# Performance work log

Measured on AMD Instinct MI355X. Metric: run time of the kernel, lower is better.

## Reference

```python
import jax, jax.numpy as jnp
import numpy as np

N_NODES = 100000
IN_CH, HID_CH, OUT_CH = 128, 128, 64
N_EDGES = 1600000


def _gcn_conv(x, W, b, src, dst, num_nodes):
    """PyG GCNConv with gcn_norm(add_self_loops=True): adds one self-loop per
    node to the given edge set, symmetric deg^-1/2 normalization, then
    gather-scale-scatter of the linearly transformed features."""
    loop = jnp.arange(num_nodes)
    s = jnp.concatenate([src, loop])
    d = jnp.concatenate([dst, loop])
    # degree over targets (flow source_to_target), edge weights = 1
    deg = jax.ops.segment_sum(jnp.ones_like(s, x.dtype), d, num_segments=num_nodes)
    dinv = jnp.where(deg > 0, deg ** -0.5, 0.0)
    norm = dinv[s] * dinv[d]                      # [E']
    h = x @ W                                     # [N, out]
    msg = h[s] * norm[:, None]                    # [E', out] gather + scale
    out = jax.ops.segment_sum(msg, d, num_segments=num_nodes)  # scatter-add
    return out + b


def setup_inputs() -> dict:
    key = jax.random.key(0)
    k = jax.random.split(key, 6)
    x = jax.random.normal(k[0], (N_NODES, IN_CH), dtype=jnp.float32)
    edge_index = jax.random.randint(k[1], (2, N_EDGES), 0, N_NODES, dtype=jnp.int64)
    # Glorot-scale params
    W1 = jax.random.normal(k[2], (IN_CH, HID_CH), dtype=jnp.float32) * (2.0 / (IN_CH + HID_CH)) ** 0.5
    b1 = jnp.zeros((HID_CH,), dtype=jnp.float32)
    W2 = jax.random.normal(k[3], (HID_CH, OUT_CH), dtype=jnp.float32) * (2.0 / (HID_CH + OUT_CH)) ** 0.5
    b2 = jnp.zeros((OUT_CH,), dtype=jnp.float32)
    return {"x": x, "edge_index": edge_index, "W1": W1, "b1": b1, "W2": W2, "b2": b2}


def reference(x, edge_index, W1, b1, W2, b2):
    num_nodes = x.shape[0]
    loop = jnp.arange(num_nodes, dtype=edge_index.dtype)
    # wrapper-level add_self_loops (GCNConv adds another internally)
    src = jnp.concatenate([edge_index[0], loop])
    dst = jnp.concatenate([edge_index[1], loop])
    h = _gcn_conv(x, W1, b1, src, dst, num_nodes)
    h = jax.nn.relu(h)
    h = _gcn_conv(h, W2, b2, src, dst, num_nodes)
    return jax.nn.log_softmax(h, axis=1)
```

## Files before the change

kernel.cpp:

```cpp
#include <hip/hip_runtime.h>
#include <cstdint>
#include <cstddef>

#define IN_CH 128
#define HID_CH 128
#define OUT_CH 64
#define BSH 8
#define PB 4096

typedef unsigned int uint32;
typedef unsigned char uchar;
typedef short bf16x8 __attribute__((ext_vector_type(8)));
typedef float f32x4 __attribute__((ext_vector_type(4)));
typedef float f32x2 __attribute__((ext_vector_type(2)));

static __device__ __forceinline__ unsigned short f2bf(float f) {
    uint32 u = __float_as_uint(f);
    u += 0x7fffu + ((u >> 16) & 1u);
    return (unsigned short)(u >> 16);
}
static __device__ __forceinline__ uchar f2fp8(float f) {
    int p = __builtin_amdgcn_cvt_pk_fp8_f32(f, f, 0, false);
    return (uchar)(p & 0xff);
}


__global__ __launch_bounds__(256) void bhist_wtrans(
    const int* __restrict__ dst, int* __restrict__ bcnt, int E, int NB, int gP,
    const float* __restrict__ W1, const float* __restrict__ W2,
    unsigned short* __restrict__ W1t, unsigned short* __restrict__ W2t) {
    if (blockIdx.x >= (uint32)gP) {
        int t = (blockIdx.x - gP) * 256 + threadIdx.x;
        if (t < 128 * 128) {
            int nc = t >> 7, k = t & 127;
            W1t[t] = f2bf(W1[k * 128 + nc]);
        }
        int u = t - 128 * 128;
        if (u >= 0 && u < 64 * 128) {
            int nc = u >> 7, k = u & 127;
            W2t[u] = f2bf(W2[k * 64 + nc]);
        }
        return;
    }
    __shared__ int h[512];
    int t = threadIdx.x;
    int e0 = blockIdx.x * PB;
    int cnt = min(PB, E - e0);
    for (int b = t; b < NB; b += 256) h[b] = 0;
    __syncthreads();
    for (int i = t; i < cnt; i += 256)
        atomicAdd(&h[dst[e0 + i] >> BSH], 1);
    __syncthreads();
    for (int b = t; b < NB; b += 256)
        if (h[b]) atomicAdd(&bcnt[b], h[b]);
}

__global__ void bscan(const int* __restrict__ bcnt, int* __restrict__ bbase,
                      int* __restrict__ bcur, int NB, int E) {
    __shared__ int s[512];
    int t = threadIdx.x;
    int v = (t < NB) ? bcnt[t] : 0;
    s[t] = v;
    __syncthreads();
    for (int o = 1; o < 512; o <<= 1) {
        int add = (t >= o) ? s[t - o] : 0;
        __syncthreads();
        s[t] += add;
        __syncthreads();
    }
    if (t < NB) { bbase[t] = s[t] - v; bcur[t] = 0; }
    if (t == 0) bbase[NB] = E;
}

__global__ __launch_bounds__(256) void part1(
    const int* __restrict__ src, const int* __restrict__ dst,
    const int* __restrict__ bbase, int* __restrict__ bcur,
    int2* __restrict__ pairBuf, int E, int NB) {
    __shared__ int2 pairs[PB];
    __shared__ int hist[512];
    __shared__ int base[512];
    int t = threadIdx.x;
    int e0 = blockIdx.x * PB;
    int cnt = min(PB, E - e0);
    for (int b = t; b < NB; b += 256) hist[b] = 0;
    __syncthreads();
    for (int i = t; i < cnt; i += 256) {
        int s = src[e0 + i], d = dst[e0 + i];
        pairs[i] = make_int2(s, d);
        atomicAdd(&hist[d >> BSH], 1);
    }
    __syncthreads();
    for (int b = t; b < NB; b += 256) {
        int h = hist[b];
        int gb = (h > 0) ? atomicAdd(&bcur[b], h) : 0;
        base[b] = bbase[b] + gb;
        hist[b] = 0;
    }
    __syncthreads();
    for (int i = t; i < cnt; i += 256) {
        int2 p = pairs[i];
        int b = p.y >> BSH;
        int q = base[b] + atomicAdd(&hist[b], 1);
        pairBuf[q] = p;
    }
}

__global__ __launch_bounds__(256) void bucket_build(
    const int2* __restrict__ pairBuf, const int* __restrict__ bbase,
    int* __restrict__ rowptr, int* __restrict__ deg, float* __restrict__ dinv,
    int* __restrict__ csr, int N) {
    __shared__ int cnt[256];
    __shared__ int loc[256];
    int b = blockIdx.x, t = threadIdx.x;
    int start = bbase[b], end = bbase[b + 1];
    cnt[t] = 0;
    __syncthreads();
    for (int i = start + t; i < end; i += 256)
        atomicAdd(&cnt[pairBuf[i].y & 255], 1);
    __syncthreads();
    int v = cnt[t];
    loc[t] = v;
    __syncthreads();
    for (int o = 1; o < 256; o <<= 1) {
        int add = (t >= o) ? loc[t - o] : 0;
        __syncthreads();
        loc[t] += add;
        __syncthreads();
    }
    int excl = loc[t] - v;
    int node = (b << BSH) + t;
    if (node < N) {
        rowptr[node] = start + excl;
        deg[node] = v;
        dinv[node] = rsqrtf((float)(v + 2));
    }
    __syncthreads();
    cnt[t] = excl;
    __syncthreads();
    for (int i = start + t; i < end; i += 256) {
        int2 p = pairBuf[i];
        int q = start + atomicAdd(&cnt[p.y & 255], 1);
        csr[q] = p.x;
    }
}


template <int OUT, bool AFP32>
__global__ __launch_bounds__(256) void gemm_mfma(
    const void* __restrict__ Av, const unsigned short* __restrict__ Wt,
    const float* __restrict__ dinv, uchar* __restrict__ C, int n) {
    constexpr int AP = 72;
    constexpr int WP = 136;
    constexpr int NT = OUT / 16;
    __shared__ unsigned short As[128 * AP];
    __shared__ unsigned short Ws[OUT * WP];

    const int t = threadIdx.x;
    const int row0 = blockIdx.x * 128;

    for (int i = t; i < OUT * 16; i += 256) {
        int rr = i >> 4, sq = i & 15;
        *(uint4*)&Ws[rr * WP + sq * 8] = *(const uint4*)(Wt + rr * 128 + sq * 8);
    }

    const int w = t >> 6, l = t & 63;
    const int q = l >> 4, r16 = l & 15;
    const int mbase = w * 32;

    f32x4 acc0[NT], acc1[NT];
    for (int i = 0; i < NT; i++) {
        acc0[i] = (f32x4){0.f, 0.f, 0.f, 0.f};
        acc1[i] = (f32x4){0.f, 0.f, 0.f, 0.f};
    }

    for (int half = 0; half < 2; half++) {
        if (half) __syncthreads();
        if (AFP32) {
            const float* A = (const float*)Av;
            for (int i = t; i < 128 * 16; i += 256) {
                int rr = i >> 4, fq = i & 15;
                float4 v = make_float4(0.f, 0.f, 0.f, 0.f);
                if (row0 + rr < n)
                    v = *(const float4*)(A + (size_t)(row0 + rr) * 128 + half * 64 + fq * 4);
                unsigned short* p = &As[rr * AP + fq * 4];
                p[0] = f2bf(v.x); p[1] = f2bf(v.y); p[2] = f2bf(v.z); p[3] = f2bf(v.w);
            }
        } else {
            const unsigned short* A = (const unsigned short*)Av;
            for (int i = t; i < 128 * 8; i += 256) {
                int rr = i >> 3, sq = i & 7;
                uint4 v = make_uint4(0, 0, 0, 0);
                if (row0 + rr < n)
                    v = *(const uint4*)(A + (size_t)(row0 + rr) * 128 + half * 64 + sq * 8);
                *(uint4*)&As[rr * AP + sq * 8] = v;
            }
        }
        __syncthreads();

#pragma unroll
        for (int kc = 0; kc < 2; kc++) {
            int ko = kc * 32 + q * 8;
            int kow = half * 64 + ko;
            bf16x8 a0 = *(const bf16x8*)&As[(mbase + r16) * AP + ko];
            bf16x8 a1 = *(const bf16x8*)&As[(mbase + 16 + r16) * AP + ko];
#pragma unroll
            for (int nt = 0; nt < NT; nt++) {
                bf16x8 b = *(const bf16x8*)&Ws[(nt * 16 + r16) * WP + kow];
                acc0[nt] = __builtin_amdgcn_mfma_f32_16x16x32_bf16(a0, b, acc0[nt], 0, 0, 0);
                acc1[nt] = __builtin_amdgcn_mfma_f32_16x16x32_bf16(a1, b, acc1[nt], 0, 0, 0);
            }
        }
    }

    float dva[4], dvb[4];
#pragma unroll
    for (int p = 0; p < 4; p++) {
        int rr = row0 + mbase + q * 4 + p;
        dva[p] = (rr < n) ? dinv[rr] : 0.f;
        dvb[p] = (rr + 16 < n) ? dinv[rr + 16] : 0.f;
    }

#pragma unroll
    for (int nt = 0; nt < NT; nt++) {
#pragma unroll
        for (int p = 0; p < 4; p++) {
            int rr = row0 + mbase + q * 4 + p;
            if (rr < n) C[(size_t)rr * OUT + nt * 16 + r16] = f2fp8(acc0[nt][p] * dva[p]);
            if (rr + 16 < n) C[(size_t)(rr + 16) * OUT + nt * 16 + r16] = f2fp8(acc1[nt][p] * dvb[p]);
        }
    }
}


__global__ __launch_bounds__(256) void agg_relu_128(
    const uchar* __restrict__ H, const int* __restrict__ csr,
    const int* __restrict__ rowptr, const int* __restrict__ deg,
    const float* __restrict__ dinv, const float* __restrict__ bias,
    unsigned short* __restrict__ out, int n) {
    int v = blockIdx.x * 16 + (threadIdx.x >> 4);
    int hl = threadIdx.x & 15;
    int gsel = threadIdx.x & 48;
    bool valid = v < n;
    int vc = valid ? v : 0;
    int base = rowptr[vc];
    int cnt = valid ? deg[vc] : 0;
    const uint32 co = (uint32)(hl * 8);

    f32x2 A0 = (f32x2){0.f, 0.f}, A1 = A0, A2 = A0, A3 = A0;
    f32x2 B0 = A0, B1 = A0, B2 = A0, B3 = A0;

#define ACC128(h, s0, s1, s2, s3)                                   \
    {                                                               \
        s0 += __builtin_amdgcn_cvt_pk_f32_fp8((h).x, false);        \
        s1 += __builtin_amdgcn_cvt_pk_f32_fp8((h).x, true);         \
        s2 += __builtin_amdgcn_cvt_pk_f32_fp8((h).y, false);        \
        s3 += __builtin_amdgcn_cvt_pk_f32_fp8((h).y, true);         \
    }

    for (int j0 = 0; j0 < cnt; j0 += 16) {
        int nj = min(16, cnt - j0);
        int ul = 0;
        if (hl < nj) ul = csr[base + j0 + hl];
        int j = 0;
        for (; j + 8 <= nj; j += 8) {
            int u0 = __shfl(ul, (j + 0) | gsel), u1 = __shfl(ul, (j + 1) | gsel);
            int u2 = __shfl(ul, (j + 2) | gsel), u3 = __shfl(ul, (j + 3) | gsel);
            int u4 = __shfl(ul, (j + 4) | gsel), u5 = __shfl(ul, (j + 5) | gsel);
            int u6 = __shfl(ul, (j + 6) | gsel), u7 = __shfl(ul, (j + 7) | gsel);
            uint2 h0 = *(const uint2*)(H + (((uint32)u0 << 7) + co));
            uint2 h1 = *(const uint2*)(H + (((uint32)u1 << 7) + co));
            uint2 h2 = *(const uint2*)(H + (((uint32)u2 << 7) + co));
            uint2 h3 = *(const uint2*)(H + (((uint32)u3 << 7) + co));
            uint2 h4 = *(const uint2*)(H + (((uint32)u4 << 7) + co));
            uint2 h5 = *(const uint2*)(H + (((uint32)u5 << 7) + co));
            uint2 h6 = *(const uint2*)(H + (((uint32)u6 << 7) + co));
            uint2 h7 = *(const uint2*)(H + (((uint32)u7 << 7) + co));
            ACC128(h0, A0, A1, A2, A3);
            ACC128(h1, B0, B1, B2, B3);
            ACC128(h2, A0, A1, A2, A3);
            ACC128(h3, B0, B1, B2, B3);
            ACC128(h4, A0, A1, A2, A3);
            ACC128(h5, B0, B1, B2, B3);
            ACC128(h6, A0, A1, A2, A3);
            ACC128(h7, B0, B1, B2, B3);
        }
        for (; j + 4 <= nj; j += 4) {
            int u0 = __shfl(ul, (j + 0) | gsel), u1 = __shfl(ul, (j + 1) | gsel);
            int u2 = __shfl(ul, (j + 2) | gsel), u3 = __shfl(ul, (j + 3) | gsel);
            uint2 h0 = *(const uint2*)(H + (((uint32)u0 << 7) + co));
            uint2 h1 = *(const uint2*)(H + (((uint32)u1 << 7) + co));
            uint2 h2 = *(const uint2*)(H + (((uint32)u2 << 7) + co));
            uint2 h3 = *(const uint2*)(H + (((uint32)u3 << 7) + co));
            ACC128(h0, A0, A1, A2, A3);
            ACC128(h1, B0, B1, B2, B3);
            ACC128(h2, A0, A1, A2, A3);
            ACC128(h3, B0, B1, B2, B3);
        }
        for (; j < nj; j++) {
            int u = __shfl(ul, j | gsel);
            uint2 h = *(const uint2*)(H + (((uint32)u << 7) + co));
            ACC128(h, A0, A1, A2, A3);
        }
    }
#undef ACC128

    if (valid) {
        float dv = dinv[vc];
        uint2 hv = *(const uint2*)(H + (((uint32)vc << 7) + co));
        f32x2 s0 = __builtin_amdgcn_cvt_pk_f32_fp8(hv.x, false);
        f32x2 s1 = __builtin_amdgcn_cvt_pk_f32_fp8(hv.x, true);
        f32x2 s2 = __builtin_amdgcn_cvt_pk_f32_fp8(hv.y, false);
        f32x2 s3 = __builtin_amdgcn_cvt_pk_f32_fp8(hv.y, true);
        const f32x2* bp = (const f32x2*)(bias + hl * 8);
        f32x2 e0 = dv * ((A0 + B0) + 2.f * s0) + bp[0];
        f32x2 e1 = dv * ((A1 + B1) + 2.f * s1) + bp[1];
        f32x2 e2 = dv * ((A2 + B2) + 2.f * s2) + bp[2];
        f32x2 e3 = dv * ((A3 + B3) + 2.f * s3) + bp[3];
        float o0 = fmaxf(e0[0], 0.f), o1 = fmaxf(e0[1], 0.f);
        float o2 = fmaxf(e1[0], 0.f), o3 = fmaxf(e1[1], 0.f);
        float o4 = fmaxf(e2[0], 0.f), o5 = fmaxf(e2[1], 0.f);
        float o6 = fmaxf(e3[0], 0.f), o7 = fmaxf(e3[1], 0.f);
        uint4 pk;
        pk.x = (uint32)f2bf(o0) | ((uint32)f2bf(o1) << 16);
        pk.y = (uint32)f2bf(o2) | ((uint32)f2bf(o3) << 16);
        pk.z = (uint32)f2bf(o4) | ((uint32)f2bf(o5) << 16);
        pk.w = (uint32)f2bf(o6) | ((uint32)f2bf(o7) << 16);
        *(uint4*)(out + (size_t)vc * 128 + hl * 8) = pk;
    }
}

__global__ __launch_bounds__(256) void agg_lsm_64(
    const uchar* __restrict__ H, const int* __restrict__ csr,
    const int* __restrict__ rowptr, const int* __restrict__ deg,
    const float* __restrict__ dinv, const float* __restrict__ bias,
    float* __restrict__ out, int n) {
    int v = blockIdx.x * 16 + (threadIdx.x >> 4);
    int hl = threadIdx.x & 15;
    int gsel = threadIdx.x & 48;
    bool valid = v < n;
    int vc = valid ? v : 0;
    int base = rowptr[vc];
    int cnt = valid ? deg[vc] : 0;
    const uint32 co = (uint32)(hl * 4);

    f32x2 A0 = (f32x2){0.f, 0.f}, A1 = A0, B0 = A0, B1 = A0;

#define ACC64(h, s0, s1)                                            \
    {                                                               \
        s0 += __builtin_amdgcn_cvt_pk_f32_fp8((h), false);          \
        s1 += __builtin_amdgcn_cvt_pk_f32_fp8((h), true);           \
    }

    for (int j0 = 0; j0 < cnt; j0 += 16) {
        int nj = min(16, cnt - j0);
        int ul = 0;
        if (hl < nj) ul = csr[base + j0 + hl];
        int j = 0;
        for (; j + 8 <= nj; j += 8) {
            int u0 = __shfl(ul, (j + 0) | gsel), u1 = __shfl(ul, (j + 1) | gsel);
            int u2 = __shfl(ul, (j + 2) | gsel), u3 = __shfl(ul, (j + 3) | gsel);
            int u4 = __shfl(ul, (j + 4) | gsel), u5 = __shfl(ul, (j + 5) | gsel);
            int u6 = __shfl(ul, (j + 6) | gsel), u7 = __shfl(ul, (j + 7) | gsel);
            uint32 h0 = *(const uint32*)(H + (((uint32)u0 << 6) + co));
            uint32 h1 = *(const uint32*)(H + (((uint32)u1 << 6) + co));
            uint32 h2 = *(const uint32*)(H + (((uint32)u2 << 6) + co));
            uint32 h3 = *(const uint32*)(H + (((uint32)u3 << 6) + co));
            uint32 h4 = *(const uint32*)(H + (((uint32)u4 << 6) + co));
            uint32 h5 = *(const uint32*)(H + (((uint32)u5 << 6) + co));
            uint32 h6 = *(const uint32*)(H + (((uint32)u6 << 6) + co));
            uint32 h7 = *(const uint32*)(H + (((uint32)u7 << 6) + co));
            ACC64(h0, A0, A1);
            ACC64(h1, B0, B1);
            ACC64(h2, A0, A1);
            ACC64(h3, B0, B1);
            ACC64(h4, A0, A1);
            ACC64(h5, B0, B1);
            ACC64(h6, A0, A1);
            ACC64(h7, B0, B1);
        }
        for (; j + 4 <= nj; j += 4) {
            int u0 = __shfl(ul, (j + 0) | gsel), u1 = __shfl(ul, (j + 1) | gsel);
            int u2 = __shfl(ul, (j + 2) | gsel), u3 = __shfl(ul, (j + 3) | gsel);
            uint32 h0 = *(const uint32*)(H + (((uint32)u0 << 6) + co));
            uint32 h1 = *(const uint32*)(H + (((uint32)u1 << 6) + co));
            uint32 h2 = *(const uint32*)(H + (((uint32)u2 << 6) + co));
            uint32 h3 = *(const uint32*)(H + (((uint32)u3 << 6) + co));
            ACC64(h0, A0, A1);
            ACC64(h1, B0, B1);
            ACC64(h2, A0, A1);
            ACC64(h3, B0, B1);
        }
        for (; j < nj; j++) {
            int u = __shfl(ul, j | gsel);
            uint32 h = *(const uint32*)(H + (((uint32)u << 6) + co));
            ACC64(h, A0, A1);
        }
    }
#undef ACC64

    float dv = dinv[vc];
    uint32 hv = *(const uint32*)(H + (((uint32)vc << 6) + co));
    f32x2 s0 = __builtin_amdgcn_cvt_pk_f32_fp8(hv, false);
    f32x2 s1 = __builtin_amdgcn_cvt_pk_f32_fp8(hv, true);
    const f32x2* bp = (const f32x2*)(bias + hl * 4);
    f32x2 w0 = dv * ((A0 + B0) + 2.f * s0) + bp[0];
    f32x2 w1 = dv * ((A1 + B1) + 2.f * s1) + bp[1];
    float v0 = w0[0], v1 = w0[1], v2 = w1[0], v3 = w1[1];
    float m = fmaxf(fmaxf(v0, v1), fmaxf(v2, v3));
    for (int o = 8; o > 0; o >>= 1) m = fmaxf(m, __shfl_xor(m, o));
    float e = (__expf(v0 - m) + __expf(v1 - m)) + (__expf(v2 - m) + __expf(v3 - m));
    for (int o = 8; o > 0; o >>= 1) e += __shfl_xor(e, o);
    float ls = m + __logf(e);
    if (valid)
        *(float4*)(out + (size_t)vc * 64 + hl * 4) =
            make_float4(v0 - ls, v1 - ls, v2 - ls, v3 - ls);
}


extern "C" void kernel_launch(void* const* d_in, const int* in_sizes, int n_in,
                              void* d_out, int out_size, void* d_ws, size_t ws_size,
                              hipStream_t stream) {
    const float* x  = (const float*)d_in[0];
    const int*   ei = (const int*)d_in[1];
    const float* W1 = (const float*)d_in[2];
    const float* b1 = (const float*)d_in[3];
    const float* W2 = (const float*)d_in[4];
    const float* b2 = (const float*)d_in[5];
    float* out = (float*)d_out;

    const int N = in_sizes[0] / IN_CH;
    const int E = in_sizes[1] / 2;
    const int* src = ei;
    const int* dst = ei + E;
    const int NB = (N + 255) >> BSH;

    char* w = (char*)d_ws;
    size_t off = 0;
    auto alloc = [&](size_t bytes) -> char* {
        char* p = w + off;
        off = (off + bytes + 255) & ~(size_t)255;
        return p;
    };
    int*   deg    = (int*)alloc((size_t)N * 4);
    int*   rowptr = (int*)alloc((size_t)N * 4);
    int*   bcnt   = (int*)alloc(512 * 4);
    int*   bbase  = (int*)alloc(513 * 4);
    int*   bcur   = (int*)alloc(512 * 4);
    float* dinv   = (float*)alloc((size_t)N * 4);
    int*   csr    = (int*)alloc((size_t)E * 4);
    unsigned short* W1t = (unsigned short*)alloc(128 * 128 * 2);
    unsigned short* W2t = (unsigned short*)alloc(64 * 128 * 2);
    uchar* H1  = (uchar*)alloc((size_t)N * HID_CH);
    unsigned short* A1b = (unsigned short*)alloc((size_t)N * HID_CH * 2);
    uchar* H2  = H1;
    int2*  pairBuf = (int2*)A1b;

    hipMemsetAsync(bcnt, 0, 512 * 4, stream);

    int gP = (E + PB - 1) / PB;

    bhist_wtrans<<<gP + 96, 256, 0, stream>>>(dst, bcnt, E, NB, gP, W1, W2, W1t, W2t);
    bscan<<<1, 512, 0, stream>>>(bcnt, bbase, bcur, NB, E);
    part1<<<gP, 256, 0, stream>>>(src, dst, bbase, bcur, pairBuf, E, NB);
    bucket_build<<<NB, 256, 0, stream>>>(pairBuf, bbase, rowptr, deg, dinv, csr, N);

    gemm_mfma<128, true><<<(N + 127) / 128, 256, 0, stream>>>(x, W1t, dinv, H1, N);
    agg_relu_128<<<(N + 15) / 16, 256, 0, stream>>>(H1, csr, rowptr, deg, dinv, b1, A1b, N);
    gemm_mfma<64, false><<<(N + 127) / 128, 256, 0, stream>>>(A1b, W2t, dinv, H2, N);
    agg_lsm_64<<<(N + 15) / 16, 256, 0, stream>>>(H2, csr, rowptr, deg, dinv, b2, out, N);
}
```

Baseline: 261.6 us.

## Load GEMM A operands directly from global into registers, drop LDS staging

```diff
diff --git a/kernel.cpp b/kernel.cpp
--- a/kernel.cpp
+++ b/kernel.cpp
@@ -146,13 +146,11 @@
 
 
 template <int OUT, bool AFP32>
-__global__ __launch_bounds__(256) void gemm_mfma(
+__global__ __launch_bounds__(256, 4) void gemm_mfma(
     const void* __restrict__ Av, const unsigned short* __restrict__ Wt,
     const float* __restrict__ dinv, uchar* __restrict__ C, int n) {
-    constexpr int AP = 72;
     constexpr int WP = 136;
     constexpr int NT = OUT / 16;
-    __shared__ unsigned short As[128 * AP];
     __shared__ unsigned short Ws[OUT * WP];
 
     const int t = threadIdx.x;
@@ -162,10 +160,16 @@
         int rr = i >> 4, sq = i & 15;
         *(uint4*)&Ws[rr * WP + sq * 8] = *(const uint4*)(Wt + rr * 128 + sq * 8);
     }
+    __syncthreads();
 
     const int w = t >> 6, l = t & 63;
     const int q = l >> 4, r16 = l & 15;
     const int mbase = w * 32;
+
+    const int ra = row0 + mbase + r16;
+    const int rb = ra + 16;
+    const int rac = min(ra, n - 1);
+    const int rbc = min(rb, n - 1);
 
     f32x4 acc0[NT], acc1[NT];
     for (int i = 0; i < NT; i++) {
@@ -173,42 +177,34 @@
         acc1[i] = (f32x4){0.f, 0.f, 0.f, 0.f};
     }
 
-    for (int half = 0; half < 2; half++) {
-        if (half) __syncthreads();
+#pragma unroll
+    for (int s = 0; s < 4; s++) {
+        const int k0 = s * 32 + q * 8;
+        bf16x8 a0, a1;
         if (AFP32) {
             const float* A = (const float*)Av;
-            for (int i = t; i < 128 * 16; i += 256) {
-                int rr = i >> 4, fq = i & 15;
-                float4 v = make_float4(0.f, 0.f, 0.f, 0.f);
-                if (row0 + rr < n)
-                    v = *(const float4*)(A + (size_t)(row0 + rr) * 128 + half * 64 + fq * 4);
-                unsigned short* p = &As[rr * AP + fq * 4];
-                p[0] = f2bf(v.x); p[1] = f2bf(v.y); p[2] = f2bf(v.z); p[3] = f2bf(v.w);
-            }
+            float4 v0 = *(const float4*)(A + (size_t)rac * 128 + k0);
+            float4 v1 = *(const float4*)(A + (size_t)rac * 128 + k0 + 4);
+            float4 u0 = *(const float4*)(A + (size_t)rbc * 128 + k0);
+            float4 u1 = *(const float4*)(A + (size_t)rbc * 128 + k0 + 4);
+            a0[0] = (short)f2bf(v0.x); a0[1] = (short)f2bf(v0.y);
+            a0[2] = (short)f2bf(v0.z); a0[3] = (short)f2bf(v0.w);
+            a0[4] = (short)f2bf(v1.x); a0[5] = (short)f2bf(v1.y);
+            a0[6] = (short)f2bf(v1.z); a0[7] = (short)f2bf(v1.w);
+            a1[0] = (short)f2bf(u0.x); a1[1] = (short)f2bf(u0.y);
+            a1[2] = (short)f2bf(u0.z); a1[3] = (short)f2bf(u0.w);
+            a1[4] = (short)f2bf(u1.x); a1[5] = (short)f2bf(u1.y);
+            a1[6] = (short)f2bf(u1.z); a1[7] = (short)f2bf(u1.w);
         } else {
             const unsigned short* A = (const unsigned short*)Av;
-            for (int i = t; i < 128 * 8; i += 256) {
-                int rr = i >> 3, sq = i & 7;
-                uint4 v = make_uint4(0, 0, 0, 0);
-                if (row0 + rr < n)
-                    v = *(const uint4*)(A + (size_t)(row0 + rr) * 128 + half * 64 + sq * 8);
-                *(uint4*)&As[rr * AP + sq * 8] = v;
-            }
-        }
-        __syncthreads();
-
+            a0 = *(const bf16x8*)(A + (size_t)rac * 128 + k0);
+            a1 = *(const bf16x8*)(A + (size_t)rbc * 128 + k0);
+        }
 #pragma unroll
-        for (int kc = 0; kc < 2; kc++) {
-            int ko = kc * 32 + q * 8;
-            int kow = half * 64 + ko;
-            bf16x8 a0 = *(const bf16x8*)&As[(mbase + r16) * AP + ko];
-            bf16x8 a1 = *(const bf16x8*)&As[(mbase + 16 + r16) * AP + ko];
-#pragma unroll
-            for (int nt = 0; nt < NT; nt++) {
-                bf16x8 b = *(const bf16x8*)&Ws[(nt * 16 + r16) * WP + kow];
-                acc0[nt] = __builtin_amdgcn_mfma_f32_16x16x32_bf16(a0, b, acc0[nt], 0, 0, 0);
-                acc1[nt] = __builtin_amdgcn_mfma_f32_16x16x32_bf16(a1, b, acc1[nt], 0, 0, 0);
-            }
+        for (int nt = 0; nt < NT; nt++) {
+            bf16x8 b = *(const bf16x8*)&Ws[(nt * 16 + r16) * WP + k0];
+            acc0[nt] = __builtin_amdgcn_mfma_f32_16x16x32_bf16(a0, b, acc0[nt], 0, 0, 0);
+            acc1[nt] = __builtin_amdgcn_mfma_f32_16x16x32_bf16(a1, b, acc1[nt], 0, 0, 0);
         }
     }
 
```

Measured after the change: 246.7 us. 1.06x faster.
